# Performance work log

Measured on AMD Instinct MI355X. Metric: run time of the kernel, lower is better.

Reference implementation:

```python
import jax, jax.numpy as jnp
import numpy as np

B, S, D, H = 2, 2048, 1024, 16
HD = D // H  # head_dim = 64
ROPE_BASE = 10000.0


def _rope_cos_sin(seq_len, head_dim, dtype):
    inv_freq = 1.0 / (ROPE_BASE ** (jnp.arange(0, head_dim, 2, dtype=jnp.float32) / head_dim))
    t = jnp.arange(seq_len, dtype=jnp.float32)
    freqs = jnp.einsum('i,j->ij', t, inv_freq)            # [S, HD/2]
    emb = jnp.concatenate([freqs, freqs], axis=-1)        # [S, HD]
    return jnp.cos(emb).astype(dtype), jnp.sin(emb).astype(dtype)


def _rotate_half(x):
    x1, x2 = jnp.split(x, 2, axis=-1)
    return jnp.concatenate([-x2, x1], axis=-1)


def setup_inputs() -> dict:
    key = jax.random.key(0)
    ks = jax.random.split(key, 5)
    scale = 1.0 / np.sqrt(D)
    x = jax.random.normal(ks[0], (B, S, D), dtype=jnp.float32)
    wq = jax.random.normal(ks[1], (D, D), dtype=jnp.float32) * scale
    wk = jax.random.normal(ks[2], (D, D), dtype=jnp.float32) * scale
    wv = jax.random.normal(ks[3], (D, D), dtype=jnp.float32) * scale
    wo = jax.random.normal(ks[4], (D, D), dtype=jnp.float32) * scale
    # causal additive mask: 0 on/below diagonal, -1e9 above
    causal = jnp.triu(jnp.full((S, S), -1e9, dtype=jnp.float32), k=1)
    attention_mask = causal[None, None, :, :]
    return {'x': x, 'attention_mask': attention_mask, 'wq': wq, 'wk': wk, 'wv': wv, 'wo': wo}


def reference(x, attention_mask, wq, wk, wv, wo):
    b, s, d = x.shape
    scale = 1.0 / np.sqrt(HD)
    # projections (torch Linear: y = x @ W.T)
    q = (x @ wq.T).reshape(b, s, H, HD).transpose(0, 2, 1, 3)  # [B,H,S,HD]
    k = (x @ wk.T).reshape(b, s, H, HD).transpose(0, 2, 1, 3)
    v = (x @ wv.T).reshape(b, s, H, HD).transpose(0, 2, 1, 3)
    cos, sin = _rope_cos_sin(s, HD, x.dtype)                   # [S, HD]
    cos = cos[None, None]
    sin = sin[None, None]
    q = q * cos + _rotate_half(q) * sin
    k = k * cos + _rotate_half(k) * sin
    scores = jnp.einsum('bhqd,bhkd->bhqk', q, k) * scale       # [B,H,S,S]
    scores = scores + attention_mask
    probs = jax.nn.softmax(scores, axis=-1)
    out = jnp.einsum('bhqk,bhkd->bhqd', probs, v)              # [B,H,S,HD]
    out = out.transpose(0, 2, 1, 3).reshape(b, s, d)
    return out @ wo.T
```

## Files before the change

### kernel.cpp

```cpp
#include <hip/hip_runtime.h>
#include <cstdint>
#include <cstddef>

typedef __attribute__((ext_vector_type(8))) _Float16 half8;
typedef __attribute__((ext_vector_type(4))) _Float16 half4;
typedef __attribute__((ext_vector_type(4))) float f32x4;

#define NB 2
#define NS 2048
#define ND 1024
#define NH 16
#define NHD 64
#define NM (NB * NS)

__device__ __forceinline__ void cvt8(const float* __restrict__ s,
                                     _Float16* __restrict__ d, int g) {
  const float4* s4 = (const float4*)s + (size_t)g * 2;
  float4 a = s4[0], b = s4[1];
  half8 h;
  h[0] = (_Float16)a.x; h[1] = (_Float16)a.y;
  h[2] = (_Float16)a.z; h[3] = (_Float16)a.w;
  h[4] = (_Float16)b.x; h[5] = (_Float16)b.y;
  h[6] = (_Float16)b.z; h[7] = (_Float16)b.w;
  *(half8*)(d + (size_t)g * 8) = h;
}

__global__ void prep(const float* __restrict__ x,
                     const float* __restrict__ wq, const float* __restrict__ wk,
                     const float* __restrict__ wv, const float* __restrict__ wo,
                     _Float16* __restrict__ xb,
                     _Float16* __restrict__ wqb, _Float16* __restrict__ wkb,
                     _Float16* __restrict__ wvb, _Float16* __restrict__ wob,
                     float* __restrict__ cosT, float* __restrict__ sinT) {
  int i = blockIdx.x * 256 + threadIdx.x;
  if (i < 524288) {
    cvt8(x, xb, i);
  } else if (i < 1048576) {
    int j = i - 524288;
    int k = j >> 17, g = j & 131071;
    const float* ws = (k == 0) ? wq : (k == 1) ? wk : (k == 2) ? wv : wo;
    _Float16* wd = (k == 0) ? wqb : (k == 1) ? wkb : (k == 2) ? wvb : wob;
    cvt8(ws, wd, g);
  } else if (i < 1056768) {
    int t0 = (i - 1048576) * 8;
#pragma unroll
    for (int e = 0; e < 8; ++e) {
      int t = t0 + e;
      int s = t >> 5, j = t & 31;
      float inv = expf(-(float)(2 * j) * (9.210340371976184f / 64.0f));
      float ang = (float)s * inv;
      cosT[t] = cosf(ang);
      sinT[t] = sinf(ang);
    }
  }
}

__device__ __forceinline__ void gload_lds16(const void* g, void* lds) {
  __builtin_amdgcn_global_load_lds(
      (const __attribute__((address_space(1))) unsigned int*)g,
      (__attribute__((address_space(3))) unsigned int*)lds, 16, 0, 0);
}

__device__ __forceinline__ float exp2_fast(float x) {
  float r;
  asm("v_exp_f32 %0, %1" : "=v"(r) : "v"(x));
  return r;
}

__device__ __forceinline__ void gemm_mainloop(const _Float16* __restrict__ A,
                                              const _Float16* __restrict__ Bw,
                                              _Float16* As, _Float16* Bs,
                                              int brow, int bcol,
                                              int lane, int wid,
                                              f32x4 acc[4][4]) {
  const int l15 = lane & 15, l4 = lane >> 4;
  const int wr = wid >> 1, wc = wid & 1;
  const int srow = lane >> 2, scol = (lane & 3) * 8;
  const _Float16* Ab = A + (size_t)(brow + srow) * ND + scol;
  const _Float16* Bb = Bw + (size_t)(bcol + srow) * ND + scol;

  for (int kt = 0; kt < ND / 32; ++kt) {
    const int k0 = kt * 32;
#pragma unroll
    for (int c = 0; c < 2; ++c) {
      const int chunk = wid * 2 + c;
      gload_lds16(Ab + (size_t)chunk * 16 * ND + k0, As + chunk * 512);
      gload_lds16(Bb + (size_t)chunk * 16 * ND + k0, Bs + chunk * 512);
    }
    __syncthreads();
    half8 af[4], bf[4];
#pragma unroll
    for (int m = 0; m < 4; ++m)
      af[m] = *(const half8*)(As + (wr * 64 + m * 16 + l15) * 32 + l4 * 8);
#pragma unroll
    for (int n = 0; n < 4; ++n)
      bf[n] = *(const half8*)(Bs + (wc * 64 + n * 16 + l15) * 32 + l4 * 8);
#pragma unroll
    for (int m = 0; m < 4; ++m)
#pragma unroll
      for (int n = 0; n < 4; ++n)
        acc[m][n] = __builtin_amdgcn_mfma_f32_16x16x32_f16(af[m], bf[n],
                                                           acc[m][n], 0, 0, 0);
    __syncthreads();
  }
}

__launch_bounds__(256, 2)
__global__ void qkv_gemm(const _Float16* __restrict__ X,
                         const _Float16* __restrict__ Wq,
                         const _Float16* __restrict__ Wk,
                         const _Float16* __restrict__ Wv,
                         _Float16* __restrict__ Qb,
                         _Float16* __restrict__ Kb,
                         _Float16* __restrict__ Vt,
                         const float* __restrict__ cosT,
                         const float* __restrict__ sinT) {
  __shared__ __align__(16) _Float16 As[128 * 32];
  __shared__ __align__(16) _Float16 Bs[128 * 32];
  const int tid = threadIdx.x, lane = tid & 63, wid = tid >> 6;
  const int l15 = lane & 15, l4 = lane >> 4;
  const int wr = wid >> 1, wc = wid & 1;
  const int brow = blockIdx.y * 128, bcol = blockIdx.x * 128;
  const int mode = blockIdx.z;
  const _Float16* W = (mode == 0) ? Wq : (mode == 1 ? Wk : Wv);

  f32x4 acc[4][4] = {};
  gemm_mainloop(X, W, As, Bs, brow, bcol, lane, wid, acc);

  const int b = brow >> 11;
  const int sbase = (brow & (NS - 1)) + wr * 64;
  const int h = (bcol >> 6) + wc;

  if (mode < 2) {
    _Float16* oh = ((mode == 0) ? Qb : Kb) + (size_t)(b * NH + h) * NS * NHD;
#pragma unroll
    for (int m = 0; m < 4; ++m) {
#pragma unroll
      for (int r = 0; r < 4; ++r) {
        const int s = sbase + m * 16 + l4 * 4 + r;
#pragma unroll
        for (int n = 0; n < 2; ++n) {
          const int hd = n * 16 + l15;
          const float c = cosT[s * 32 + hd];
          const float sn = sinT[s * 32 + hd];
          const float lo = acc[m][n][r], hi = acc[m][n + 2][r];
          oh[(size_t)s * NHD + hd]      = (_Float16)(lo * c - hi * sn);
          oh[(size_t)s * NHD + hd + 32] = (_Float16)(hi * c + lo * sn);
        }
      }
    }
  } else {
#pragma unroll
    for (int m = 0; m < 4; ++m) {
      const int s0 = sbase + m * 16 + l4 * 4;
#pragma unroll
      for (int n = 0; n < 4; ++n) {
        const int hd = n * 16 + l15;
        half4 pk;
        pk[0] = (_Float16)acc[m][n][0];
        pk[1] = (_Float16)acc[m][n][1];
        pk[2] = (_Float16)acc[m][n][2];
        pk[3] = (_Float16)acc[m][n][3];
        *(half4*)(Vt + ((size_t)(b * NH + h) * NHD + hd) * NS + s0) = pk;
      }
    }
  }
}

__launch_bounds__(256, 4)
__global__ void flash_attn(const _Float16* __restrict__ Qb,
                           const _Float16* __restrict__ Kb,
                           const _Float16* __restrict__ Vt,
                           _Float16* __restrict__ Ob) {
  __shared__ __align__(16) _Float16 Ks[2][64 * 64];
  __shared__ __align__(16) _Float16 Vs[2][64 * 64];
  const int tid = threadIdx.x, lane = tid & 63, wid = tid >> 6;
  const int l15 = lane & 15, l4 = lane >> 4;
  const int bh = blockIdx.x & 31, pr = blockIdx.x >> 5;
  const _Float16* Qh = Qb + (size_t)bh * NS * NHD;
  const char* Kg = (const char*)(Kb + (size_t)bh * NS * NHD);
  const char* Vg = (const char*)(Vt + (size_t)bh * NHD * NS);

  const float K1 = 0.125f * 1.4426950408889634f;
  const int swz_lane = ((lane >> 3) & 7) << 4;
  const int qloc = wid * 16 + l15;
  const int rswz = (l15 & 7) << 4;
  const int b = bh >> 4, h = bh & 15;

  for (int item = 0; item < 2; ++item) {
    const int qt = item ? pr : 31 - pr;

    half8 qf[2];
#pragma unroll
    for (int kk = 0; kk < 2; ++kk)
      qf[kk] = *(const half8*)&Qh[(size_t)(qt * 64 + wid * 16 + l15) * NHD + kk * 32 + l4 * 8];

    f32x4 oacc[4] = {};
    float mrun = -3.0e38f, lrun = 0.f;
    const int nkt = qt + 1;

#pragma unroll
    for (int c = 0; c < 2; ++c) {
      const int chunk = wid * 2 + c;
      const int slot = chunk * 1024 + lane * 16;
      const int sw = slot ^ swz_lane;
      gload_lds16(Kg + sw, (char*)&Ks[0][0] + slot);
      const int vrow = slot >> 7;
      gload_lds16(Vg + (size_t)vrow * (NS * 2) + (sw & 127), (char*)&Vs[0][0] + slot);
    }
    __syncthreads();

    int cur = 0;
    for (int kt = 0; kt < nkt; ++kt) {
      if (kt + 1 < nkt) {
        const size_t knext = (size_t)(kt + 1);
#pragma unroll
        for (int c = 0; c < 2; ++c) {
          const int chunk = wid * 2 + c;
          const int slot = chunk * 1024 + lane * 16;
          const int sw = slot ^ swz_lane;
          gload_lds16(Kg + knext * 8192 + sw, (char*)&Ks[cur ^ 1][0] + slot);
          const int vrow = slot >> 7;
          gload_lds16(Vg + (size_t)vrow * (NS * 2) + knext * 128 + (sw & 127),
                      (char*)&Vs[cur ^ 1][0] + slot);
        }
      }

      const bool diag = (kt == qt);
      const char* Kbuf = (const char*)&Ks[cur][0];
      const char* Vbuf = (const char*)&Vs[cur][0];

      f32x4 sacc[4] = {};
      __builtin_amdgcn_s_setprio(1);
#pragma unroll
      for (int kk = 0; kk < 2; ++kk) {
#pragma unroll
        for (int n = 0; n < 4; ++n) {
          if (diag && n > wid) continue;
          const int off = ((n * 16 + l15) * 128 + kk * 64 + l4 * 16) ^ rswz;
          half8 kf = *(const half8*)(Kbuf + off);
          sacc[n] = __builtin_amdgcn_mfma_f32_16x16x32_f16(kf, qf[kk], sacc[n], 0, 0, 0);
        }
      }
      __builtin_amdgcn_s_setprio(0);

      float t[16];
#pragma unroll
      for (int n = 0; n < 4; ++n)
#pragma unroll
        for (int r = 0; r < 4; ++r) {
          float v = sacc[n][r] * K1;
          if (diag) {
            const int ki = n * 16 + l4 * 4 + r;
            v = (ki > qloc) ? -3.0e38f : v;
          }
          t[n * 4 + r] = v;
        }
      float mx = t[0];
#pragma unroll
      for (int j = 1; j < 16; ++j) mx = fmaxf(mx, t[j]);
      mx = fmaxf(mx, __shfl_xor(mx, 16, 64));
      mx = fmaxf(mx, __shfl_xor(mx, 32, 64));
      const float mnew = fmaxf(mrun, mx);
      const float alpha = exp2_fast(mrun - mnew);
      mrun = mnew;
      float ps[16], rs = 0.f;
#pragma unroll
      for (int j = 0; j < 16; ++j) {
        ps[j] = exp2_fast(t[j] - mnew);
        rs += ps[j];
      }
      rs += __shfl_xor(rs, 16, 64);
      rs += __shfl_xor(rs, 32, 64);
      lrun = lrun * alpha + rs;
#pragma unroll
      for (int n = 0; n < 4; ++n) {
        oacc[n][0] *= alpha; oacc[n][1] *= alpha;
        oacc[n][2] *= alpha; oacc[n][3] *= alpha;
      }

      __builtin_amdgcn_s_setprio(1);
#pragma unroll
      for (int c = 0; c < 2; ++c) {
        if (diag && c == 1 && wid < 2) continue;
        half8 pb;
#pragma unroll
        for (int j = 0; j < 8; ++j)
          pb[j] = (_Float16)ps[(2 * c + (j >> 2)) * 4 + (j & 3)];
#pragma unroll
        for (int n = 0; n < 4; ++n) {
          const int off0 = ((n * 16 + l15) * 128 + c * 64 + l4 * 8) ^ rswz;
          const int off1 = off0 ^ 32;
          half4 vlo = *(const half4*)(Vbuf + off0);
          half4 vhi = *(const half4*)(Vbuf + off1);
          half8 va;
          va[0] = vlo[0]; va[1] = vlo[1]; va[2] = vlo[2]; va[3] = vlo[3];
          va[4] = vhi[0]; va[5] = vhi[1]; va[6] = vhi[2]; va[7] = vhi[3];
          oacc[n] = __builtin_amdgcn_mfma_f32_16x16x32_f16(va, pb, oacc[n], 0, 0, 0);
        }
      }
      __builtin_amdgcn_s_setprio(0);

      __syncthreads();
      cur ^= 1;
    }

    const int s = qt * 64 + wid * 16 + l15;
    const float invl = 1.0f / lrun;
#pragma unroll
    for (int n = 0; n < 4; ++n) {
      half4 o;
      o[0] = (_Float16)(oacc[n][0] * invl);
      o[1] = (_Float16)(oacc[n][1] * invl);
      o[2] = (_Float16)(oacc[n][2] * invl);
      o[3] = (_Float16)(oacc[n][3] * invl);
      *(half4*)&Ob[((size_t)(b * NS + s)) * ND + h * NHD + n * 16 + l4 * 4] = o;
    }
  }
}

__launch_bounds__(256, 2)
__global__ void proj_gemm(const _Float16* __restrict__ A,
                          const _Float16* __restrict__ W,
                          float* __restrict__ out) {
  __shared__ __align__(16) _Float16 As[128 * 32];
  __shared__ __align__(16) _Float16 Bs[128 * 32];
  const int tid = threadIdx.x, lane = tid & 63, wid = tid >> 6;
  const int l15 = lane & 15, l4 = lane >> 4;
  const int wr = wid >> 1, wc = wid & 1;
  const int brow = blockIdx.y * 128, bcol = blockIdx.x * 128;
  f32x4 acc[4][4] = {};
  gemm_mainloop(A, W, As, Bs, brow, bcol, lane, wid, acc);
#pragma unroll
  for (int m = 0; m < 4; ++m)
#pragma unroll
    for (int n = 0; n < 4; ++n)
#pragma unroll
      for (int r = 0; r < 4; ++r)
        out[(size_t)(brow + wr * 64 + m * 16 + l4 * 4 + r) * ND
            + bcol + wc * 64 + n * 16 + l15] = acc[m][n][r];
}

extern "C" void kernel_launch(void* const* d_in, const int* in_sizes, int n_in,
                              void* d_out, int out_size, void* d_ws, size_t ws_size,
                              hipStream_t stream) {
  const float* x  = (const float*)d_in[0];
  const float* wq = (const float*)d_in[2];
  const float* wk = (const float*)d_in[3];
  const float* wv = (const float*)d_in[4];
  const float* wo = (const float*)d_in[5];
  float* out = (float*)d_out;

  char* w = (char*)d_ws;
  _Float16* xb   = (_Float16*)(w);
  _Float16* wqb  = (_Float16*)(w + (8ull  << 20));
  _Float16* wkb  = (_Float16*)(w + (10ull << 20));
  _Float16* wvb  = (_Float16*)(w + (12ull << 20));
  _Float16* wob  = (_Float16*)(w + (14ull << 20));
  _Float16* Qb   = (_Float16*)(w + (16ull << 20));
  _Float16* Kb   = (_Float16*)(w + (24ull << 20));
  _Float16* Vt   = (_Float16*)(w + (32ull << 20));
  _Float16* Ob   = (_Float16*)(w + (40ull << 20));
  float*    cosT = (float*)   (w + (48ull << 20));
  float*    sinT = (float*)   (w + (48ull << 20) + (1ull << 18));

  dim3 blk(256);
  prep<<<4128, blk, 0, stream>>>(x, wq, wk, wv, wo, xb, wqb, wkb, wvb, wob,
                                 cosT, sinT);
  qkv_gemm<<<dim3(8, 32, 3), blk, 0, stream>>>(xb, wqb, wkb, wvb, Qb, Kb, Vt,
                                               cosT, sinT);
  flash_attn<<<512, blk, 0, stream>>>(Qb, Kb, Vt, Ob);
  proj_gemm<<<dim3(8, 32), blk, 0, stream>>>(Ob, wob, out);
}
```

Baseline: 109.5 us.

## Retile output projection to 128x64 blocks and trim softmax arithmetic in attention

```diff
diff --git a/kernel.cpp b/kernel.cpp
--- a/kernel.cpp
+++ b/kernel.cpp
@@ -4,6 +4,7 @@
 
 typedef __attribute__((ext_vector_type(8))) _Float16 half8;
 typedef __attribute__((ext_vector_type(4))) _Float16 half4;
+typedef __attribute__((ext_vector_type(2))) __fp16 fp16x2;
 typedef __attribute__((ext_vector_type(4))) float f32x4;
 
 #define NB 2
@@ -189,6 +190,7 @@
 
   for (int item = 0; item < 2; ++item) {
     const int qt = item ? pr : 31 - pr;
+    const int nkt = qt + 1;
 
     half8 qf[2];
 #pragma unroll
@@ -197,7 +199,6 @@
 
     f32x4 oacc[4] = {};
     float mrun = -3.0e38f, lrun = 0.f;
-    const int nkt = qt + 1;
 
 #pragma unroll
     for (int c = 0; c < 2; ++c) {
@@ -244,40 +245,38 @@
       }
       __builtin_amdgcn_s_setprio(0);
 
-      float t[16];
+      float traw[16];
 #pragma unroll
       for (int n = 0; n < 4; ++n)
 #pragma unroll
         for (int r = 0; r < 4; ++r) {
-          float v = sacc[n][r] * K1;
+          float v = sacc[n][r];
           if (diag) {
             const int ki = n * 16 + l4 * 4 + r;
             v = (ki > qloc) ? -3.0e38f : v;
           }
-          t[n * 4 + r] = v;
-        }
-      float mx = t[0];
-#pragma unroll
-      for (int j = 1; j < 16; ++j) mx = fmaxf(mx, t[j]);
+          traw[n * 4 + r] = v;
+        }
+      float mx = traw[0];
+#pragma unroll
+      for (int j = 1; j < 16; ++j) mx = fmaxf(mx, traw[j]);
       mx = fmaxf(mx, __shfl_xor(mx, 16, 64));
       mx = fmaxf(mx, __shfl_xor(mx, 32, 64));
+      mx *= K1;
       const float mnew = fmaxf(mrun, mx);
       const float alpha = exp2_fast(mrun - mnew);
       mrun = mnew;
       float ps[16], rs = 0.f;
 #pragma unroll
       for (int j = 0; j < 16; ++j) {
-        ps[j] = exp2_fast(t[j] - mnew);
+        ps[j] = exp2_fast(__builtin_fmaf(traw[j], K1, -mnew));
         rs += ps[j];
       }
       rs += __shfl_xor(rs, 16, 64);
       rs += __shfl_xor(rs, 32, 64);
       lrun = lrun * alpha + rs;
 #pragma unroll
-      for (int n = 0; n < 4; ++n) {
-        oacc[n][0] *= alpha; oacc[n][1] *= alpha;
-        oacc[n][2] *= alpha; oacc[n][3] *= alpha;
-      }
+      for (int n = 0; n < 4; ++n) oacc[n] *= alpha;
 
       __builtin_amdgcn_s_setprio(1);
 #pragma unroll
@@ -285,8 +284,12 @@
         if (diag && c == 1 && wid < 2) continue;
         half8 pb;
 #pragma unroll
-        for (int j = 0; j < 8; ++j)
-          pb[j] = (_Float16)ps[(2 * c + (j >> 2)) * 4 + (j & 3)];
+        for (int q2 = 0; q2 < 4; ++q2) {
+          fp16x2 pp = __builtin_amdgcn_cvt_pkrtz(ps[8 * c + 2 * q2],
+                                                 ps[8 * c + 2 * q2 + 1]);
+          pb[2 * q2]     = (_Float16)pp[0];
+          pb[2 * q2 + 1] = (_Float16)pp[1];
+        }
 #pragma unroll
         for (int n = 0; n < 4; ++n) {
           const int off0 = ((n * 16 + l15) * 128 + c * 64 + l4 * 8) ^ rswz;
@@ -309,11 +312,12 @@
     const float invl = 1.0f / lrun;
 #pragma unroll
     for (int n = 0; n < 4; ++n) {
+      f32x4 ov = oacc[n] * invl;
       half4 o;
-      o[0] = (_Float16)(oacc[n][0] * invl);
-      o[1] = (_Float16)(oacc[n][1] * invl);
-      o[2] = (_Float16)(oacc[n][2] * invl);
-      o[3] = (_Float16)(oacc[n][3] * invl);
+      o[0] = (_Float16)ov[0];
+      o[1] = (_Float16)ov[1];
+      o[2] = (_Float16)ov[2];
+      o[3] = (_Float16)ov[3];
       *(half4*)&Ob[((size_t)(b * NS + s)) * ND + h * NHD + n * 16 + l4 * 4] = o;
     }
   }
@@ -324,21 +328,48 @@
                           const _Float16* __restrict__ W,
                           float* __restrict__ out) {
   __shared__ __align__(16) _Float16 As[128 * 32];
-  __shared__ __align__(16) _Float16 Bs[128 * 32];
+  __shared__ __align__(16) _Float16 Bs[64 * 32];
   const int tid = threadIdx.x, lane = tid & 63, wid = tid >> 6;
   const int l15 = lane & 15, l4 = lane >> 4;
   const int wr = wid >> 1, wc = wid & 1;
-  const int brow = blockIdx.y * 128, bcol = blockIdx.x * 128;
-  f32x4 acc[4][4] = {};
-  gemm_mainloop(A, W, As, Bs, brow, bcol, lane, wid, acc);
+  const int brow = blockIdx.y * 128, bcol = blockIdx.x * 64;
+  const int srow = lane >> 2, scol = (lane & 3) * 8;
+  const _Float16* Ab = A + (size_t)(brow + srow) * ND + scol;
+  const _Float16* Bb = W + (size_t)(bcol + srow) * ND + scol;
+
+  f32x4 acc[4][2] = {};
+  for (int kt = 0; kt < ND / 32; ++kt) {
+    const int k0 = kt * 32;
+#pragma unroll
+    for (int c = 0; c < 2; ++c) {
+      const int chunk = wid * 2 + c;
+      gload_lds16(Ab + (size_t)chunk * 16 * ND + k0, As + chunk * 512);
+    }
+    gload_lds16(Bb + (size_t)wid * 16 * ND + k0, Bs + wid * 512);
+    __syncthreads();
+    half8 af[4], bf[2];
+#pragma unroll
+    for (int m = 0; m < 4; ++m)
+      af[m] = *(const half8*)(As + (wr * 64 + m * 16 + l15) * 32 + l4 * 8);
+#pragma unroll
+    for (int n = 0; n < 2; ++n)
+      bf[n] = *(const half8*)(Bs + (wc * 32 + n * 16 + l15) * 32 + l4 * 8);
+#pragma unroll
+    for (int m = 0; m < 4; ++m)
+#pragma unroll
+      for (int n = 0; n < 2; ++n)
+        acc[m][n] = __builtin_amdgcn_mfma_f32_16x16x32_f16(af[m], bf[n],
+                                                           acc[m][n], 0, 0, 0);
+    __syncthreads();
+  }
 #pragma unroll
   for (int m = 0; m < 4; ++m)
 #pragma unroll
-    for (int n = 0; n < 4; ++n)
+    for (int n = 0; n < 2; ++n)
 #pragma unroll
       for (int r = 0; r < 4; ++r)
         out[(size_t)(brow + wr * 64 + m * 16 + l4 * 4 + r) * ND
-            + bcol + wc * 64 + n * 16 + l15] = acc[m][n][r];
+            + bcol + wc * 32 + n * 16 + l15] = acc[m][n][r];
 }
 
 extern "C" void kernel_launch(void* const* d_in, const int* in_sizes, int n_in,
@@ -370,5 +401,5 @@
   qkv_gemm<<<dim3(8, 32, 3), blk, 0, stream>>>(xb, wqb, wkb, wvb, Qb, Kb, Vt,
                                                cosT, sinT);
   flash_attn<<<512, blk, 0, stream>>>(Qb, Kb, Vt, Ob);
-  proj_gemm<<<dim3(8, 32), blk, 0, stream>>>(Ob, wob, out);
-}
+  proj_gemm<<<dim3(16, 32), blk, 0, stream>>>(Ob, wob, out);
+}
```

After: 107.9 us. No clear change (-1.4%).
